# Performance work log

Measured on AMD Instinct MI355X. Metric: run time of the kernel, lower is better.

The kernel has to match this reference:

```python
import jax, jax.numpy as jnp
import numpy as np

B, H, L, D = 16, 8, 512, 64
TEMPERATURE = 8.0  # sqrt(d_k)
MASK_SENTINEL = -10000.0
BIG_NEG = 1e9


def setup_inputs() -> dict:
    key = jax.random.key(0)
    kq, kk, kv, km = jax.random.split(key, 4)
    q = jax.random.normal(kq, (B * H, L, D), dtype=jnp.float32)
    k = jax.random.normal(kk, (B * H, L, D), dtype=jnp.float32)
    v = jax.random.normal(kv, (B * H, L, D), dtype=jnp.float32)
    mask = jnp.where(jax.random.bernoulli(km, 0.1, (B, L)), MASK_SENTINEL, 0.0).astype(jnp.float32)
    return {"q": q, "k": k, "v": v, "mask": mask, "n_head": H}


def reference(q, k, v, mask, n_head):
    # attn: [B*H, L, L]
    attn = jnp.einsum("bid,bjd->bij", q, k) / TEMPERATURE
    # masked_fill(mask == -10000, 1e9); other values subtracted as-is
    m = jnp.where(mask == MASK_SENTINEL, BIG_NEG, mask)          # [B, L]
    m_bh = jnp.repeat(m, n_head, axis=0)                          # [B*H, L], matches reshape(B*H, ...)
    # row mask (mask.unsqueeze(-1).repeat) and its transpose (column mask)
    attn = attn - m_bh[:, :, None] - m_bh[:, None, :]
    attn = jax.nn.softmax(attn, axis=2)
    # dropout in eval mode (identity) for the deterministic reference
    output = jnp.einsum("bij,bjd->bid", attn, v)
    return output, attn
```

## Files before the change

kernel.cpp:

```cpp
#include <hip/hip_runtime.h>
#include <stdint.h>

#define Ln 512
#define Dn 64
#define BHn 128
#define AOFF ((size_t)BHn*Ln*Dn)

typedef __attribute__((ext_vector_type(8))) short short8;
typedef __attribute__((ext_vector_type(4))) float f32x4;
typedef __attribute__((ext_vector_type(4))) unsigned int u32x4;
typedef __attribute__((ext_vector_type(2))) unsigned int u32x2;

#define KSTR 72
#define VTSTR 136

__device__ __forceinline__ uint16_t f2bf(float f){
  uint32_t x = __float_as_uint(f);
  return (uint16_t)((x + 0x7FFFu + ((x>>16)&1u)) >> 16);
}
__device__ __forceinline__ float bf2f(uint16_t u){ return __uint_as_float(((uint32_t)u)<<16); }
__device__ __forceinline__ uint32_t pack2(float a, float b){
  return (uint32_t)f2bf(a) | ((uint32_t)f2bf(b)<<16);
}

extern "C" __global__ __launch_bounds__(256, 2)
void attn_mfma(const float* __restrict__ qg, const float* __restrict__ kg,
               const float* __restrict__ vg, const float* __restrict__ mg,
               float* __restrict__ outg)
{
  __shared__ uint4 ldsraw[(36864 + 2048)/16];
  uint16_t* KHI = (uint16_t*)ldsraw;
  uint16_t* KLO = KHI + 128*KSTR;
  uint16_t* VT  = (uint16_t*)ldsraw;
  float*    CMV = (float*)((char*)ldsraw + 36864);

  const int t    = threadIdx.x;
  const int lane = t & 63;
  const int wv   = t >> 6;
  const int li   = lane & 15;
  const int lq   = lane >> 4;
  const int bh   = blockIdx.y;
  const int b    = bh >> 3;
  const int i0   = blockIdx.x*64 + wv*16;
  const size_t base = (size_t)bh * (Ln*Dn);
  const float* mrow = mg + b*Ln;

  {
    float m0 = mrow[t], m1 = mrow[t+256];
    CMV[t]     = (m0 < -9000.f) ? 1e9f : m0;
    CMV[t+256] = (m1 < -9000.f) ? 1e9f : m1;
  }

  short8 qhi[2], qlo[2];
  {
    const float* qrow = qg + base + (size_t)(i0 + li)*Dn;
    #pragma unroll
    for (int kt=0; kt<2; ++kt){
      const float* p = qrow + kt*32 + lq*8;
      f32x4 x0 = *(const f32x4*)p;
      f32x4 x1 = *(const f32x4*)(p+4);
      #pragma unroll
      for (int e=0; e<8; ++e){
        float x = (e<4) ? x0[e] : x1[e-4];
        uint16_t h = f2bf(x);
        qhi[kt][e] = (short)h;
        qlo[kt][e] = (short)f2bf(x - bf2f(h));
      }
    }
  }

  f32x4 acc[32];
  #pragma unroll
  for (int j=0; j<32; ++j) acc[j] = (f32x4)0.f;

  const int sj = t>>1, skh = t&1;
  #pragma unroll
  for (int c=0; c<4; ++c){
    __syncthreads();
    {
      const float* kr = kg + base + (size_t)(c*128 + sj)*Dn + skh*32;
      uint16_t* dhi = KHI + sj*KSTR + skh*32;
      uint16_t* dlo = KLO + sj*KSTR + skh*32;
      #pragma unroll
      for (int w2=0; w2<4; ++w2){
        f32x4 x0 = *(const f32x4*)(kr + w2*8);
        f32x4 x1 = *(const f32x4*)(kr + w2*8 + 4);
        uint32_t hw[4], lw[4];
        #pragma unroll
        for (int pi=0; pi<4; ++pi){
          float a0 = (pi<2) ? x0[pi*2]   : x1[(pi-2)*2];
          float a1 = (pi<2) ? x0[pi*2+1] : x1[(pi-2)*2+1];
          uint16_t h0 = f2bf(a0), h1 = f2bf(a1);
          hw[pi] = (uint32_t)h0 | ((uint32_t)h1<<16);
          lw[pi] = (uint32_t)f2bf(a0 - bf2f(h0)) | ((uint32_t)f2bf(a1 - bf2f(h1))<<16);
        }
        *(u32x4*)(dhi + w2*8) = (u32x4){hw[0],hw[1],hw[2],hw[3]};
        *(u32x4*)(dlo + w2*8) = (u32x4){lw[0],lw[1],lw[2],lw[3]};
      }
    }
    __syncthreads();
    #pragma unroll
    for (int jt=0; jt<8; ++jt){
      #pragma unroll
      for (int kt=0; kt<2; ++kt){
        const int off = (jt*16 + li)*KSTR + kt*32 + lq*8;
        short8 kh = *(const short8*)(KHI + off);
        short8 kl = *(const short8*)(KLO + off);
        f32x4 A = acc[c*8+jt];
        A = __builtin_amdgcn_mfma_f32_16x16x32_bf16(qhi[kt], kh, A, 0,0,0);
        A = __builtin_amdgcn_mfma_f32_16x16x32_bf16(qhi[kt], kl, A, 0,0,0);
        A = __builtin_amdgcn_mfma_f32_16x16x32_bf16(qlo[kt], kh, A, 0,0,0);
        acc[c*8+jt] = A;
      }
    }
  }

  float rml[4];
  #pragma unroll
  for (int e=0; e<4; ++e){
    float mv = mrow[i0 + lq*4 + e];
    rml[e] = (mv < -9000.f) ? 1e9f : mv;
  }
  #pragma unroll
  for (int j=0; j<32; ++j){
    float cm = CMV[j*16 + li];
    #pragma unroll
    for (int e=0; e<4; ++e){
      float s = acc[j][e]*0.125f - rml[e];
      acc[j][e] = s - cm;
    }
  }
  float* attn_base = outg + AOFF + (size_t)bh*Ln*Ln;
  #pragma unroll
  for (int e=0; e<4; ++e){
    const int row = i0 + lq*4 + e;
    float mx = -3.4e38f;
    #pragma unroll
    for (int j=0; j<32; ++j) mx = fmaxf(mx, acc[j][e]);
    #pragma unroll
    for (int sh=1; sh<16; sh<<=1) mx = fmaxf(mx, __shfl_xor(mx, sh));
    float sum = 0.f;
    #pragma unroll
    for (int j=0; j<32; ++j){ float ee = __expf(acc[j][e]-mx); acc[j][e] = ee; sum += ee; }
    #pragma unroll
    for (int sh=1; sh<16; sh<<=1) sum += __shfl_xor(sum, sh);
    const float inv = 1.0f/sum;
    #pragma unroll
    for (int j=0; j<32; ++j){
      float p = acc[j][e]*inv;
      attn_base[(size_t)row*Ln + j*16 + li] = p;
    }
  }

  asm volatile("s_waitcnt vmcnt(0)" ::: "memory");
  f32x4 oacc[4];
  #pragma unroll
  for (int dt=0; dt<4; ++dt) oacc[dt] = (f32x4)0.f;
  const float* arow = attn_base + (size_t)(i0 + li)*Ln;

  #pragma unroll
  for (int c=0; c<4; ++c){
    __syncthreads();
    #pragma unroll
    for (int it=0; it<2; ++it){
      const int j0 = (t>>4)*4 + it*64;
      const int d0 = (t&15)*4;
      const float* vr = vg + base + (size_t)(c*128 + j0)*Dn + d0;
      f32x4 r0 = *(const f32x4*)(vr);
      f32x4 r1 = *(const f32x4*)(vr + Dn);
      f32x4 r2 = *(const f32x4*)(vr + 2*Dn);
      f32x4 r3 = *(const f32x4*)(vr + 3*Dn);
      #pragma unroll
      for (int qd=0; qd<4; ++qd){
        u32x2 w; w.x = pack2(r0[qd], r1[qd]); w.y = pack2(r2[qd], r3[qd]);
        *(u32x2*)(VT + (d0+qd)*VTSTR + j0) = w;
      }
    }
    __syncthreads();
    #pragma unroll
    for (int ktl=0; ktl<4; ++ktl){
      const float* pp = arow + c*128 + ktl*32 + lq*8;
      f32x4 p0 = *(const f32x4*)pp;
      f32x4 p1 = *(const f32x4*)(pp+4);
      short8 pfrag;
      #pragma unroll
      for (int e=0; e<8; ++e) pfrag[e] = (short)f2bf((e<4) ? p0[e] : p1[e-4]);
      #pragma unroll
      for (int dt=0; dt<4; ++dt){
        short8 vb = *(const short8*)(VT + (dt*16 + li)*VTSTR + ktl*32 + lq*8);
        oacc[dt] = __builtin_amdgcn_mfma_f32_16x16x32_bf16(pfrag, vb, oacc[dt], 0,0,0);
      }
    }
  }

  #pragma unroll
  for (int dt=0; dt<4; ++dt){
    #pragma unroll
    for (int e=0; e<4; ++e){
      outg[base + (size_t)(i0 + lq*4 + e)*Dn + dt*16 + li] = oacc[dt][e];
    }
  }
}

extern "C" void kernel_launch(void* const* d_in, const int* in_sizes, int n_in,
                              void* d_out, int out_size, void* d_ws, size_t ws_size,
                              hipStream_t stream)
{
  (void)in_sizes; (void)n_in; (void)d_ws; (void)ws_size; (void)out_size;
  dim3 grid(Ln/64, BHn);
  attn_mfma<<<grid, 256, 0, stream>>>((const float*)d_in[0], (const float*)d_in[1],
                                      (const float*)d_in[2], (const float*)d_in[3],
                                      (float*)d_out);
}
```

Measured before the change: 258.1 us.

## Transpose MFMA operands so P stays in registers and stores are vectorized

Swaps the MFMA A/B operands so each lane owns four consecutive columns of a single row. The softmax reduction then needs only two cross-lane shuffles, and the attention and output rows are written with 16-byte vector stores. Probabilities are no longer read back from global memory for the PV product; they are packed to bf16 in a per-wave LDS scratch area placed after the VT region, removing the global round-trip and the vmcnt wait. The cost is some extra LDS traffic, and the scratch layout relies on offsets that must not overlap the V tile.

```diff
diff --git a/kernel.cpp b/kernel.cpp
--- a/kernel.cpp
+++ b/kernel.cpp
@@ -11,8 +11,9 @@
 typedef __attribute__((ext_vector_type(4))) unsigned int u32x4;
 typedef __attribute__((ext_vector_type(2))) unsigned int u32x2;
 
-#define KSTR 72
+#define KSTR  72
 #define VTSTR 136
+#define PSTRH 136
 
 __device__ __forceinline__ uint16_t f2bf(float f){
   uint32_t x = __float_as_uint(f);
@@ -42,8 +43,10 @@
   const int bh   = blockIdx.y;
   const int b    = bh >> 3;
   const int i0   = blockIdx.x*64 + wv*16;
-  const size_t base = (size_t)bh * (Ln*Dn);
+  const size_t base = (size_t)bh*(Ln*Dn);
   const float* mrow = mg + b*Ln;
+
+  uint16_t* PW = (uint16_t*)((char*)ldsraw + 17408 + wv*(16*PSTRH*2));
 
   {
     float m0 = mrow[t], m1 = mrow[t+256];
@@ -107,56 +110,54 @@
         short8 kh = *(const short8*)(KHI + off);
         short8 kl = *(const short8*)(KLO + off);
         f32x4 A = acc[c*8+jt];
-        A = __builtin_amdgcn_mfma_f32_16x16x32_bf16(qhi[kt], kh, A, 0,0,0);
-        A = __builtin_amdgcn_mfma_f32_16x16x32_bf16(qhi[kt], kl, A, 0,0,0);
-        A = __builtin_amdgcn_mfma_f32_16x16x32_bf16(qlo[kt], kh, A, 0,0,0);
+        A = __builtin_amdgcn_mfma_f32_16x16x32_bf16(kh, qhi[kt], A, 0,0,0);
+        A = __builtin_amdgcn_mfma_f32_16x16x32_bf16(kl, qhi[kt], A, 0,0,0);
+        A = __builtin_amdgcn_mfma_f32_16x16x32_bf16(kh, qlo[kt], A, 0,0,0);
         acc[c*8+jt] = A;
       }
     }
   }
 
-  float rml[4];
-  #pragma unroll
-  for (int e=0; e<4; ++e){
-    float mv = mrow[i0 + lq*4 + e];
-    rml[e] = (mv < -9000.f) ? 1e9f : mv;
-  }
-  #pragma unroll
-  for (int j=0; j<32; ++j){
-    float cm = CMV[j*16 + li];
-    #pragma unroll
-    for (int e=0; e<4; ++e){
-      float s = acc[j][e]*0.125f - rml[e];
-      acc[j][e] = s - cm;
-    }
-  }
-  float* attn_base = outg + AOFF + (size_t)bh*Ln*Ln;
-  #pragma unroll
-  for (int e=0; e<4; ++e){
-    const int row = i0 + lq*4 + e;
-    float mx = -3.4e38f;
-    #pragma unroll
-    for (int j=0; j<32; ++j) mx = fmaxf(mx, acc[j][e]);
-    #pragma unroll
-    for (int sh=1; sh<16; sh<<=1) mx = fmaxf(mx, __shfl_xor(mx, sh));
-    float sum = 0.f;
-    #pragma unroll
-    for (int j=0; j<32; ++j){ float ee = __expf(acc[j][e]-mx); acc[j][e] = ee; sum += ee; }
-    #pragma unroll
-    for (int sh=1; sh<16; sh<<=1) sum += __shfl_xor(sum, sh);
-    const float inv = 1.0f/sum;
-    #pragma unroll
-    for (int j=0; j<32; ++j){
-      float p = acc[j][e]*inv;
-      attn_base[(size_t)row*Ln + j*16 + li] = p;
-    }
-  }
-
-  asm volatile("s_waitcnt vmcnt(0)" ::: "memory");
+  {
+    float mv = mrow[i0 + li];
+    const float rmv = (mv < -9000.f) ? 1e9f : mv;
+    #pragma unroll
+    for (int jt=0; jt<32; ++jt){
+      f32x4 cm = *(const f32x4*)(CMV + jt*16 + lq*4);
+      #pragma unroll
+      for (int r=0; r<4; ++r)
+        acc[jt][r] = (acc[jt][r]*0.125f - rmv) - cm[r];
+    }
+  }
+  float mx = -3.4e38f;
+  #pragma unroll
+  for (int jt=0; jt<32; ++jt)
+    #pragma unroll
+    for (int r=0; r<4; ++r) mx = fmaxf(mx, acc[jt][r]);
+  mx = fmaxf(mx, __shfl_xor(mx, 16));
+  mx = fmaxf(mx, __shfl_xor(mx, 32));
+  float sum = 0.f;
+  #pragma unroll
+  for (int jt=0; jt<32; ++jt)
+    #pragma unroll
+    for (int r=0; r<4; ++r){ float e = __expf(acc[jt][r]-mx); acc[jt][r] = e; sum += e; }
+  sum += __shfl_xor(sum, 16);
+  sum += __shfl_xor(sum, 32);
+  const float inv = 1.0f/sum;
+
+  {
+    float* arow = outg + AOFF + (size_t)bh*Ln*Ln + (size_t)(i0+li)*Ln;
+    #pragma unroll
+    for (int jt=0; jt<32; ++jt){
+      f32x4 p = acc[jt]*inv;
+      acc[jt] = p;
+      *(f32x4*)(arow + jt*16 + lq*4) = p;
+    }
+  }
+
   f32x4 oacc[4];
   #pragma unroll
   for (int dt=0; dt<4; ++dt) oacc[dt] = (f32x4)0.f;
-  const float* arow = attn_base + (size_t)(i0 + li)*Ln;
 
   #pragma unroll
   for (int c=0; c<4; ++c){
@@ -178,28 +179,26 @@
     }
     __syncthreads();
     #pragma unroll
-    for (int ktl=0; ktl<4; ++ktl){
-      const float* pp = arow + c*128 + ktl*32 + lq*8;
-      f32x4 p0 = *(const f32x4*)pp;
-      f32x4 p1 = *(const f32x4*)(pp+4);
-      short8 pfrag;
-      #pragma unroll
-      for (int e=0; e<8; ++e) pfrag[e] = (short)f2bf((e<4) ? p0[e] : p1[e-4]);
+    for (int jtl=0; jtl<8; ++jtl){
+      const f32x4 p = acc[c*8+jtl];
+      u32x2 w; w.x = pack2(p[0], p[1]); w.y = pack2(p[2], p[3]);
+      *(u32x2*)(PW + li*PSTRH + jtl*16 + lq*4) = w;
+    }
+    asm volatile("s_waitcnt lgkmcnt(0)" ::: "memory");
+    #pragma unroll
+    for (int c32=0; c32<4; ++c32){
+      short8 pf = *(const short8*)(PW + li*PSTRH + c32*32 + lq*8);
       #pragma unroll
       for (int dt=0; dt<4; ++dt){
-        short8 vb = *(const short8*)(VT + (dt*16 + li)*VTSTR + ktl*32 + lq*8);
-        oacc[dt] = __builtin_amdgcn_mfma_f32_16x16x32_bf16(pfrag, vb, oacc[dt], 0,0,0);
-      }
-    }
-  }
-
-  #pragma unroll
-  for (int dt=0; dt<4; ++dt){
-    #pragma unroll
-    for (int e=0; e<4; ++e){
-      outg[base + (size_t)(i0 + lq*4 + e)*Dn + dt*16 + li] = oacc[dt][e];
-    }
-  }
+        short8 vb = *(const short8*)(VT + (dt*16+li)*VTSTR + c32*32 + lq*8);
+        oacc[dt] = __builtin_amdgcn_mfma_f32_16x16x32_bf16(vb, pf, oacc[dt], 0,0,0);
+      }
+    }
+  }
+
+  #pragma unroll
+  for (int dt=0; dt<4; ++dt)
+    *(f32x4*)(outg + base + (size_t)(i0+li)*Dn + dt*16 + lq*4) = oacc[dt];
 }
 
 extern "C" void kernel_launch(void* const* d_in, const int* in_sizes, int n_in,
```

After: 239.9 us. 1.08x faster.
